# Kernel tuning notes

Hardware: AMD Instinct MI355X
Metric: run time of the kernel (lower is better)

## Reference

```python
import jax, jax.numpy as jnp
import numpy as np

SEQ_LEN = 1024
DIM = 384
QK_DIM = 64
BATCH = 16


def setup_inputs() -> dict:
    key = jax.random.key(0)
    k_x, k_qw, k_qb, k_kw = jax.random.split(key, 4)
    bound = DIM ** (-0.5)
    x = jax.random.normal(k_x, (BATCH, SEQ_LEN, DIM), dtype=jnp.float32)
    # ColumnLinear params: weight [seq_len, out_features, in_features]
    q_weight = jax.random.uniform(k_qw, (SEQ_LEN, QK_DIM, DIM), minval=-bound, maxval=bound, dtype=jnp.float32)
    q_bias = jnp.zeros((SEQ_LEN, QK_DIM), dtype=jnp.float32)  # init zeros; keep as param
    k_weight = jax.random.uniform(k_kw, (SEQ_LEN, QK_DIM, DIM), minval=-bound, maxval=bound, dtype=jnp.float32)
    attn_bias = jnp.zeros((SEQ_LEN, SEQ_LEN), dtype=jnp.float32)
    return {"x": x, "q_weight": q_weight, "q_bias": q_bias, "k_weight": k_weight, "attn_bias": attn_bias}


def reference(x, q_weight, q_bias, k_weight, attn_bias):
    scale = DIM ** (-0.5)  # note: scale uses dim, not qk_dim
    # per-column (untied) linear projections
    q = scale * (jnp.einsum('bnc,ndc->bnd', x, q_weight) + q_bias)  # [B,S,qk]
    k = jnp.einsum('bnc,ndc->bnd', x, k_weight)                     # [B,S,qk]
    attn = jnp.einsum('bnd,bmd->bnm', q, k) + attn_bias             # [B,S,S]
    attn = jax.nn.softmax(attn, axis=-1)
    out = jnp.einsum('bnm,bmc->bnc', attn, x)                       # value = input
    return out, attn
```

## Files before the change

kernel.cpp:

```cpp
#include <hip/hip_runtime.h>

#define B_  16
#define S_  1024
#define D_  384
#define QK_ 64

typedef __attribute__((ext_vector_type(8))) short bf16x8;
typedef __attribute__((ext_vector_type(4))) short bf16x4;
typedef __attribute__((ext_vector_type(4))) float f32x4;

__device__ __forceinline__ short f2bf(float f) {
  union { float f; unsigned u; } v; v.f = f;
  unsigned r = v.u + 0x7FFFu + ((v.u >> 16) & 1u);
  return (short)(r >> 16);
}

__device__ __forceinline__ bf16x4 cvt4(const float4 v) {
  bf16x4 r;
  r[0] = f2bf(v.x); r[1] = f2bf(v.y); r[2] = f2bf(v.z); r[3] = f2bf(v.w);
  return r;
}

__global__ __launch_bounds__(256) void k_proj(
    const float* __restrict__ x, const float* __restrict__ qw,
    const float* __restrict__ qb, const float* __restrict__ kw,
    unsigned short* __restrict__ Qb, unsigned short* __restrict__ Kb) {
  __shared__ __attribute__((aligned(16))) short xs[16 * 392];
  __shared__ __attribute__((aligned(16))) short wsb[128 * 104];

  const int pos  = blockIdx.x;
  const int tid  = threadIdx.x;
  const int lane = tid & 63;
  const int w    = tid >> 6;
  const int col  = lane & 15;
  const int quad = lane >> 4;

#pragma unroll
  for (int r = 0; r < 6; ++r) {
    int li = tid + 256 * r;
    int brow = li / 96, c4 = li % 96;
    float4 v = *(const float4*)&x[(brow * S_ + pos) * D_ + 4 * c4];
    *(bf16x4*)&xs[brow * 392 + 4 * c4] = cvt4(v);
  }

  f32x4 acc0 = {0.f, 0.f, 0.f, 0.f};
  f32x4 acc1 = {0.f, 0.f, 0.f, 0.f};
  const int tt0 = 2 * w, tt1 = 2 * w + 1;

  for (int chunk = 0; chunk < 4; ++chunk) {
    const int c0 = chunk * 96;
    __syncthreads();
#pragma unroll
    for (int r = 0; r < 12; ++r) {
      int li = tid + 256 * r;
      int j = li / 24, c4 = li % 24;
      const float* src = (j < 64)
          ? &qw[(pos * 64 + j) * D_ + c0 + 4 * c4]
          : &kw[(pos * 64 + (j - 64)) * D_ + c0 + 4 * c4];
      *(bf16x4*)&wsb[j * 104 + 4 * c4] = cvt4(*(const float4*)src);
    }
    __syncthreads();
#pragma unroll
    for (int ks = 0; ks < 3; ++ks) {
      bf16x8 aF = *(const bf16x8*)&xs[col * 392 + c0 + ks * 32 + quad * 8];
      bf16x8 b0 = *(const bf16x8*)&wsb[(tt0 * 16 + col) * 104 + ks * 32 + quad * 8];
      bf16x8 b1 = *(const bf16x8*)&wsb[(tt1 * 16 + col) * 104 + ks * 32 + quad * 8];
      acc0 = __builtin_amdgcn_mfma_f32_16x16x32_bf16(aF, b0, acc0, 0, 0, 0);
      acc1 = __builtin_amdgcn_mfma_f32_16x16x32_bf16(aF, b1, acc1, 0, 0, 0);
    }
  }

  const float SCALE = 0.051031036307982884f;
#pragma unroll
  for (int a = 0; a < 2; ++a) {
    const f32x4 acc = a ? acc1 : acc0;
    const int tt = a ? tt1 : tt0;
    const int j = tt * 16 + col;
#pragma unroll
    for (int r = 0; r < 4; ++r) {
      const int brow = quad * 4 + r;
      float v = acc[r];
      if (j < 64) {
        v = SCALE * (v + qb[pos * 64 + j]);
        Qb[(brow * S_ + pos) * QK_ + j] = (unsigned short)f2bf(v);
      } else {
        Kb[(brow * S_ + pos) * QK_ + (j - 64)] = (unsigned short)f2bf(v);
      }
    }
  }
}

__global__ __launch_bounds__(256) void k_logits(
    const unsigned short* __restrict__ Qb, const unsigned short* __restrict__ Kb,
    const float* __restrict__ bias, float* __restrict__ attn) {
  __shared__ __attribute__((aligned(16))) short Qs[64 * 72];
  __shared__ __attribute__((aligned(16))) short Ks[64 * 72];
  const int gid = blockIdx.x;
  const int b = gid >> 8, it = (gid >> 4) & 15, jt = gid & 15;
  const int i0 = it * 64, j0 = jt * 64;
  const int tid = threadIdx.x, lane = tid & 63, w = tid >> 6;
  const int col = lane & 15, quad = lane >> 4;

#pragma unroll
  for (int r = 0; r < 2; ++r) {
    int li = tid + 256 * r;
    int row = li >> 3, q8 = li & 7;
    *(uint4*)&Qs[row * 72 + q8 * 8] =
        *(const uint4*)&Qb[(b * S_ + i0 + row) * QK_ + q8 * 8];
    *(uint4*)&Ks[row * 72 + q8 * 8] =
        *(const uint4*)&Kb[(b * S_ + j0 + row) * QK_ + q8 * 8];
  }
  __syncthreads();

  f32x4 acc[4] = {{0.f,0.f,0.f,0.f},{0.f,0.f,0.f,0.f},
                  {0.f,0.f,0.f,0.f},{0.f,0.f,0.f,0.f}};
#pragma unroll
  for (int ks = 0; ks < 2; ++ks) {
    bf16x8 aF = *(const bf16x8*)&Qs[(w * 16 + col) * 72 + ks * 32 + quad * 8];
#pragma unroll
    for (int s = 0; s < 4; ++s) {
      bf16x8 bF = *(const bf16x8*)&Ks[(s * 16 + col) * 72 + ks * 32 + quad * 8];
      acc[s] = __builtin_amdgcn_mfma_f32_16x16x32_bf16(aF, bF, acc[s], 0, 0, 0);
    }
  }
#pragma unroll
  for (int s = 0; s < 4; ++s) {
    const int j = j0 + s * 16 + col;
#pragma unroll
    for (int r = 0; r < 4; ++r) {
      const int i = i0 + w * 16 + quad * 4 + r;
      attn[(size_t)(b * S_ + i) * S_ + j] = acc[s][r] + bias[i * S_ + j];
    }
  }
}

__global__ __launch_bounds__(256) void k_softmax(float* __restrict__ attn) {
  const int tid = threadIdx.x, lane = tid & 63, w = tid >> 6;
  float* p = attn + (size_t)blockIdx.x * S_;
  float4 v = *(const float4*)&p[tid * 4];
  float m = fmaxf(fmaxf(v.x, v.y), fmaxf(v.z, v.w));
#pragma unroll
  for (int off = 32; off > 0; off >>= 1) m = fmaxf(m, __shfl_xor(m, off));
  __shared__ float redm[4], reds[4];
  if (lane == 0) redm[w] = m;
  __syncthreads();
  m = fmaxf(fmaxf(redm[0], redm[1]), fmaxf(redm[2], redm[3]));
  float4 e;
  e.x = __expf(v.x - m); e.y = __expf(v.y - m);
  e.z = __expf(v.z - m); e.w = __expf(v.w - m);
  float s = e.x + e.y + e.z + e.w;
#pragma unroll
  for (int off = 32; off > 0; off >>= 1) s += __shfl_xor(s, off);
  if (lane == 0) reds[w] = s;
  __syncthreads();
  s = reds[0] + reds[1] + reds[2] + reds[3];
  const float inv = 1.0f / s;
  e.x *= inv; e.y *= inv; e.z *= inv; e.w *= inv;
  *(float4*)&p[tid * 4] = e;
}

__global__ __launch_bounds__(256) void k_out(
    const float* __restrict__ attn, const float* __restrict__ x,
    float* __restrict__ out) {
  __shared__ __attribute__((aligned(16))) short Ps[64 * 40];
  __shared__ __attribute__((aligned(16))) short XsT[128 * 40];
  const int gid = blockIdx.x;
  const int b = gid / 48, r48 = gid % 48;
  const int it = r48 / 3, ct = r48 % 3;
  const int i0 = it * 64, c0 = ct * 128;
  const int tid = threadIdx.x, lane = tid & 63, w = tid >> 6;
  const int col = lane & 15, quad = lane >> 4;

  f32x4 acc[8] = {{0.f,0.f,0.f,0.f},{0.f,0.f,0.f,0.f},{0.f,0.f,0.f,0.f},
                  {0.f,0.f,0.f,0.f},{0.f,0.f,0.f,0.f},{0.f,0.f,0.f,0.f},
                  {0.f,0.f,0.f,0.f},{0.f,0.f,0.f,0.f}};

  for (int j0 = 0; j0 < S_; j0 += 32) {
    __syncthreads();
#pragma unroll
    for (int r = 0; r < 2; ++r) {
      int li = tid + 256 * r;
      int ii = li >> 3, f4 = li & 7;
      float4 v = *(const float4*)&attn[(size_t)(b * S_ + i0 + ii) * S_ + j0 + f4 * 4];
      *(bf16x4*)&Ps[ii * 40 + f4 * 4] = cvt4(v);
    }
#pragma unroll
    for (int r = 0; r < 4; ++r) {
      int li = tid + 256 * r;
      int jj = li >> 5, f4 = li & 31;
      float4 v = *(const float4*)&x[(b * S_ + j0 + jj) * D_ + c0 + f4 * 4];
      XsT[(f4 * 4 + 0) * 40 + jj] = f2bf(v.x);
      XsT[(f4 * 4 + 1) * 40 + jj] = f2bf(v.y);
      XsT[(f4 * 4 + 2) * 40 + jj] = f2bf(v.z);
      XsT[(f4 * 4 + 3) * 40 + jj] = f2bf(v.w);
    }
    __syncthreads();
    bf16x8 aF = *(const bf16x8*)&Ps[(w * 16 + col) * 40 + quad * 8];
#pragma unroll
    for (int s = 0; s < 8; ++s) {
      bf16x8 bF = *(const bf16x8*)&XsT[(s * 16 + col) * 40 + quad * 8];
      acc[s] = __builtin_amdgcn_mfma_f32_16x16x32_bf16(aF, bF, acc[s], 0, 0, 0);
    }
  }
#pragma unroll
  for (int s = 0; s < 8; ++s) {
    const int c = c0 + s * 16 + col;
#pragma unroll
    for (int r = 0; r < 4; ++r) {
      const int i = i0 + w * 16 + quad * 4 + r;
      out[(size_t)(b * S_ + i) * D_ + c] = acc[s][r];
    }
  }
}

extern "C" void kernel_launch(void* const* d_in, const int* in_sizes, int n_in,
                              void* d_out, int out_size, void* d_ws, size_t ws_size,
                              hipStream_t stream) {
  const float* x  = (const float*)d_in[0];
  const float* qw = (const float*)d_in[1];
  const float* qb = (const float*)d_in[2];
  const float* kw = (const float*)d_in[3];
  const float* ab = (const float*)d_in[4];

  float* out  = (float*)d_out;
  float* attn = out + (size_t)B_ * S_ * D_;

  unsigned short* Qb = (unsigned short*)d_ws;
  unsigned short* Kb = Qb + (size_t)B_ * S_ * QK_;

  k_proj   <<<S_,          256, 0, stream>>>(x, qw, qb, kw, Qb, Kb);
  k_logits <<<B_ * 16 * 16, 256, 0, stream>>>(Qb, Kb, ab, attn);
  k_softmax<<<B_ * S_,     256, 0, stream>>>(attn);
  k_out    <<<B_ * 16 * 3, 256, 0, stream>>>(attn, x, out);
}
```

Before: 416.8 us.

## Fuse logits and softmax, pre-transpose x to bf16, feed k_out from bf16 probabilities

The logits and softmax kernels are merged into one kernel that computes a full 16-row slab of scores in registers, applies bias, max, exp and normalization, then writes the fp32 attention plus a bf16 copy. This removes the fp32 attention round trip that the separate softmax pass did. A new prep kernel writes x transposed in bf16, so k_out loads bf16 tiles directly, with no per-iteration conversion or transposing scatter, and uses larger 64x192 tiles. The projection now streams weights straight from global into MFMA operands instead of staging them in LDS. The cost is extra workspace traffic for Xt and Pb and high register pressure in the fused kernel, which holds 16 accumulators.

```diff
diff --git a/kernel.cpp b/kernel.cpp
--- a/kernel.cpp
+++ b/kernel.cpp
@@ -15,10 +15,39 @@
   return (short)(r >> 16);
 }
 
-__device__ __forceinline__ bf16x4 cvt4(const float4 v) {
-  bf16x4 r;
-  r[0] = f2bf(v.x); r[1] = f2bf(v.y); r[2] = f2bf(v.z); r[3] = f2bf(v.w);
+__device__ __forceinline__ bf16x8 cvt8(const float4 a, const float4 b) {
+  bf16x8 r;
+  r[0] = f2bf(a.x); r[1] = f2bf(a.y); r[2] = f2bf(a.z); r[3] = f2bf(a.w);
+  r[4] = f2bf(b.x); r[5] = f2bf(b.y); r[6] = f2bf(b.z); r[7] = f2bf(b.w);
   return r;
+}
+
+__global__ __launch_bounds__(256) void k_prep(
+    const float* __restrict__ x, unsigned short* __restrict__ Xt) {
+  __shared__ __attribute__((aligned(16))) short t[64 * 72];
+  const int gid = blockIdx.x;
+  const int b = gid / 96, r96 = gid % 96;
+  const int jt = r96 / 6, ct = r96 % 6;
+  const int j0 = jt * 64, c0 = ct * 64;
+  const int tid = threadIdx.x;
+#pragma unroll
+  for (int r = 0; r < 4; ++r) {
+    int li = tid + 256 * r;
+    int jj = li >> 4, f4 = li & 15;
+    float4 v = *(const float4*)&x[(size_t)(b * S_ + j0 + jj) * D_ + c0 + f4 * 4];
+    t[(f4 * 4 + 0) * 72 + jj] = f2bf(v.x);
+    t[(f4 * 4 + 1) * 72 + jj] = f2bf(v.y);
+    t[(f4 * 4 + 2) * 72 + jj] = f2bf(v.z);
+    t[(f4 * 4 + 3) * 72 + jj] = f2bf(v.w);
+  }
+  __syncthreads();
+#pragma unroll
+  for (int r = 0; r < 2; ++r) {
+    int li = tid + 256 * r;
+    int cc = li >> 3, q8 = li & 7;
+    *(uint4*)&Xt[(size_t)(b * D_ + c0 + cc) * S_ + j0 + q8 * 8] =
+        *(const uint4*)&t[cc * 72 + q8 * 8];
+  }
 }
 
 __global__ __launch_bounds__(256) void k_proj(
@@ -26,8 +55,6 @@
     const float* __restrict__ qb, const float* __restrict__ kw,
     unsigned short* __restrict__ Qb, unsigned short* __restrict__ Kb) {
   __shared__ __attribute__((aligned(16))) short xs[16 * 392];
-  __shared__ __attribute__((aligned(16))) short wsb[128 * 104];
-
   const int pos  = blockIdx.x;
   const int tid  = threadIdx.x;
   const int lane = tid & 63;
@@ -39,171 +66,192 @@
   for (int r = 0; r < 6; ++r) {
     int li = tid + 256 * r;
     int brow = li / 96, c4 = li % 96;
-    float4 v = *(const float4*)&x[(brow * S_ + pos) * D_ + 4 * c4];
-    *(bf16x4*)&xs[brow * 392 + 4 * c4] = cvt4(v);
-  }
-
-  f32x4 acc0 = {0.f, 0.f, 0.f, 0.f};
-  f32x4 acc1 = {0.f, 0.f, 0.f, 0.f};
-  const int tt0 = 2 * w, tt1 = 2 * w + 1;
-
-  for (int chunk = 0; chunk < 4; ++chunk) {
-    const int c0 = chunk * 96;
-    __syncthreads();
-#pragma unroll
-    for (int r = 0; r < 12; ++r) {
-      int li = tid + 256 * r;
-      int j = li / 24, c4 = li % 24;
-      const float* src = (j < 64)
-          ? &qw[(pos * 64 + j) * D_ + c0 + 4 * c4]
-          : &kw[(pos * 64 + (j - 64)) * D_ + c0 + 4 * c4];
-      *(bf16x4*)&wsb[j * 104 + 4 * c4] = cvt4(*(const float4*)src);
-    }
-    __syncthreads();
-#pragma unroll
-    for (int ks = 0; ks < 3; ++ks) {
-      bf16x8 aF = *(const bf16x8*)&xs[col * 392 + c0 + ks * 32 + quad * 8];
-      bf16x8 b0 = *(const bf16x8*)&wsb[(tt0 * 16 + col) * 104 + ks * 32 + quad * 8];
-      bf16x8 b1 = *(const bf16x8*)&wsb[(tt1 * 16 + col) * 104 + ks * 32 + quad * 8];
-      acc0 = __builtin_amdgcn_mfma_f32_16x16x32_bf16(aF, b0, acc0, 0, 0, 0);
-      acc1 = __builtin_amdgcn_mfma_f32_16x16x32_bf16(aF, b1, acc1, 0, 0, 0);
-    }
+    float4 v = *(const float4*)&x[(size_t)(brow * S_ + pos) * D_ + 4 * c4];
+    bf16x4 c; c[0]=f2bf(v.x); c[1]=f2bf(v.y); c[2]=f2bf(v.z); c[3]=f2bf(v.w);
+    *(bf16x4*)&xs[brow * 392 + 4 * c4] = c;
+  }
+  __syncthreads();
+
+  const bool isQ = (w < 2);
+  const int jt0 = (w & 1) * 2;
+  const float* wp = isQ ? qw : kw;
+  const float* p0 = wp + (size_t)(pos * 64 + jt0 * 16 + col) * D_ + quad * 8;
+  const float* p1 = p0 + 16 * D_;
+
+  f32x4 acc0 = {0.f,0.f,0.f,0.f};
+  f32x4 acc1 = {0.f,0.f,0.f,0.f};
+#pragma unroll 4
+  for (int ks = 0; ks < 12; ++ks) {
+    float4 a0 = *(const float4*)(p0 + ks * 32);
+    float4 a1 = *(const float4*)(p0 + ks * 32 + 4);
+    float4 b0 = *(const float4*)(p1 + ks * 32);
+    float4 b1 = *(const float4*)(p1 + ks * 32 + 4);
+    bf16x8 aF = *(const bf16x8*)&xs[col * 392 + ks * 32 + quad * 8];
+    acc0 = __builtin_amdgcn_mfma_f32_16x16x32_bf16(aF, cvt8(a0, a1), acc0, 0, 0, 0);
+    acc1 = __builtin_amdgcn_mfma_f32_16x16x32_bf16(aF, cvt8(b0, b1), acc1, 0, 0, 0);
   }
 
   const float SCALE = 0.051031036307982884f;
 #pragma unroll
   for (int a = 0; a < 2; ++a) {
     const f32x4 acc = a ? acc1 : acc0;
-    const int tt = a ? tt1 : tt0;
-    const int j = tt * 16 + col;
+    const int j = (jt0 + a) * 16 + col;
 #pragma unroll
     for (int r = 0; r < 4; ++r) {
       const int brow = quad * 4 + r;
       float v = acc[r];
-      if (j < 64) {
+      if (isQ) {
         v = SCALE * (v + qb[pos * 64 + j]);
-        Qb[(brow * S_ + pos) * QK_ + j] = (unsigned short)f2bf(v);
+        Qb[(size_t)(brow * S_ + pos) * QK_ + j] = (unsigned short)f2bf(v);
       } else {
-        Kb[(brow * S_ + pos) * QK_ + (j - 64)] = (unsigned short)f2bf(v);
+        Kb[(size_t)(brow * S_ + pos) * QK_ + j] = (unsigned short)f2bf(v);
       }
     }
   }
 }
 
-__global__ __launch_bounds__(256) void k_logits(
+__global__ __launch_bounds__(256) void k_attn(
     const unsigned short* __restrict__ Qb, const unsigned short* __restrict__ Kb,
-    const float* __restrict__ bias, float* __restrict__ attn) {
-  __shared__ __attribute__((aligned(16))) short Qs[64 * 72];
-  __shared__ __attribute__((aligned(16))) short Ks[64 * 72];
-  const int gid = blockIdx.x;
-  const int b = gid >> 8, it = (gid >> 4) & 15, jt = gid & 15;
-  const int i0 = it * 64, j0 = jt * 64;
+    const float* __restrict__ bias, float* __restrict__ attn,
+    unsigned short* __restrict__ Pb) {
+  __shared__ float rm[4][16];
+  __shared__ float rs[4][16];
+  const int b  = blockIdx.x >> 6;
+  const int i0 = (blockIdx.x & 63) * 16;
   const int tid = threadIdx.x, lane = tid & 63, w = tid >> 6;
   const int col = lane & 15, quad = lane >> 4;
 
-#pragma unroll
-  for (int r = 0; r < 2; ++r) {
-    int li = tid + 256 * r;
-    int row = li >> 3, q8 = li & 7;
-    *(uint4*)&Qs[row * 72 + q8 * 8] =
-        *(const uint4*)&Qb[(b * S_ + i0 + row) * QK_ + q8 * 8];
-    *(uint4*)&Ks[row * 72 + q8 * 8] =
-        *(const uint4*)&Kb[(b * S_ + j0 + row) * QK_ + q8 * 8];
-  }
-  __syncthreads();
-
-  f32x4 acc[4] = {{0.f,0.f,0.f,0.f},{0.f,0.f,0.f,0.f},
-                  {0.f,0.f,0.f,0.f},{0.f,0.f,0.f,0.f}};
-#pragma unroll
-  for (int ks = 0; ks < 2; ++ks) {
-    bf16x8 aF = *(const bf16x8*)&Qs[(w * 16 + col) * 72 + ks * 32 + quad * 8];
-#pragma unroll
-    for (int s = 0; s < 4; ++s) {
-      bf16x8 bF = *(const bf16x8*)&Ks[(s * 16 + col) * 72 + ks * 32 + quad * 8];
-      acc[s] = __builtin_amdgcn_mfma_f32_16x16x32_bf16(aF, bF, acc[s], 0, 0, 0);
-    }
-  }
-#pragma unroll
-  for (int s = 0; s < 4; ++s) {
-    const int j = j0 + s * 16 + col;
-#pragma unroll
-    for (int r = 0; r < 4; ++r) {
-      const int i = i0 + w * 16 + quad * 4 + r;
-      attn[(size_t)(b * S_ + i) * S_ + j] = acc[s][r] + bias[i * S_ + j];
-    }
-  }
-}
-
-__global__ __launch_bounds__(256) void k_softmax(float* __restrict__ attn) {
-  const int tid = threadIdx.x, lane = tid & 63, w = tid >> 6;
-  float* p = attn + (size_t)blockIdx.x * S_;
-  float4 v = *(const float4*)&p[tid * 4];
-  float m = fmaxf(fmaxf(v.x, v.y), fmaxf(v.z, v.w));
-#pragma unroll
-  for (int off = 32; off > 0; off >>= 1) m = fmaxf(m, __shfl_xor(m, off));
-  __shared__ float redm[4], reds[4];
-  if (lane == 0) redm[w] = m;
-  __syncthreads();
-  m = fmaxf(fmaxf(redm[0], redm[1]), fmaxf(redm[2], redm[3]));
-  float4 e;
-  e.x = __expf(v.x - m); e.y = __expf(v.y - m);
-  e.z = __expf(v.z - m); e.w = __expf(v.w - m);
-  float s = e.x + e.y + e.z + e.w;
-#pragma unroll
-  for (int off = 32; off > 0; off >>= 1) s += __shfl_xor(s, off);
-  if (lane == 0) reds[w] = s;
-  __syncthreads();
-  s = reds[0] + reds[1] + reds[2] + reds[3];
-  const float inv = 1.0f / s;
-  e.x *= inv; e.y *= inv; e.z *= inv; e.w *= inv;
-  *(float4*)&p[tid * 4] = e;
+  const unsigned short* qrow = Qb + (size_t)(b * S_ + i0 + col) * QK_;
+  const bf16x8 aF0 = *(const bf16x8*)(qrow);
+  const bf16x8 aF1 = *(const bf16x8*)(qrow + 32);
+  const bf16x8 aQ0 = *(const bf16x8*)(qrow + quad * 8);
+  const bf16x8 aQ1 = *(const bf16x8*)(qrow + 32 + quad * 8);
+  (void)aF0; (void)aF1;
+
+  f32x4 acc[16];
+#pragma unroll
+  for (int s = 0; s < 16; ++s) acc[s] = (f32x4){0.f,0.f,0.f,0.f};
+
+  const unsigned short* kbase = Kb + (size_t)b * S_ * QK_ + (size_t)(w * 256 + col) * QK_;
+#pragma unroll 4
+  for (int s = 0; s < 16; ++s) {
+    const unsigned short* krow = kbase + (size_t)s * 16 * QK_;
+    bf16x8 b0 = *(const bf16x8*)(krow + quad * 8);
+    bf16x8 b1 = *(const bf16x8*)(krow + 32 + quad * 8);
+    acc[s] = __builtin_amdgcn_mfma_f32_16x16x32_bf16(aQ0, b0, acc[s], 0, 0, 0);
+    acc[s] = __builtin_amdgcn_mfma_f32_16x16x32_bf16(aQ1, b1, acc[s], 0, 0, 0);
+  }
+
+  float pm[4] = {-1e30f, -1e30f, -1e30f, -1e30f};
+#pragma unroll 4
+  for (int s = 0; s < 16; ++s) {
+    const int j = w * 256 + s * 16 + col;
+#pragma unroll
+    for (int r = 0; r < 4; ++r) {
+      acc[s][r] += bias[(size_t)(i0 + quad * 4 + r) * S_ + j];
+      pm[r] = fmaxf(pm[r], acc[s][r]);
+    }
+  }
+#pragma unroll
+  for (int m = 1; m < 16; m <<= 1) {
+#pragma unroll
+    for (int r = 0; r < 4; ++r) pm[r] = fmaxf(pm[r], __shfl_xor(pm[r], m));
+  }
+  if (col == 0) {
+#pragma unroll
+    for (int r = 0; r < 4; ++r) rm[w][quad * 4 + r] = pm[r];
+  }
+  __syncthreads();
+#pragma unroll
+  for (int r = 0; r < 4; ++r) {
+    const int i = quad * 4 + r;
+    pm[r] = fmaxf(fmaxf(rm[0][i], rm[1][i]), fmaxf(rm[2][i], rm[3][i]));
+  }
+
+  float ps[4] = {0.f, 0.f, 0.f, 0.f};
+#pragma unroll 4
+  for (int s = 0; s < 16; ++s) {
+#pragma unroll
+    for (int r = 0; r < 4; ++r) {
+      float e = __expf(acc[s][r] - pm[r]);
+      acc[s][r] = e;
+      ps[r] += e;
+    }
+  }
+#pragma unroll
+  for (int m = 1; m < 16; m <<= 1) {
+#pragma unroll
+    for (int r = 0; r < 4; ++r) ps[r] += __shfl_xor(ps[r], m);
+  }
+  if (col == 0) {
+#pragma unroll
+    for (int r = 0; r < 4; ++r) rs[w][quad * 4 + r] = ps[r];
+  }
+  __syncthreads();
+#pragma unroll
+  for (int r = 0; r < 4; ++r) {
+    const int i = quad * 4 + r;
+    ps[r] = 1.0f / (rs[0][i] + rs[1][i] + rs[2][i] + rs[3][i]);
+  }
+
+#pragma unroll 4
+  for (int s = 0; s < 16; ++s) {
+    const int j = w * 256 + s * 16 + col;
+#pragma unroll
+    for (int r = 0; r < 4; ++r) {
+      const size_t row = (size_t)(b * S_ + i0 + quad * 4 + r);
+      float v = acc[s][r] * ps[r];
+      attn[row * S_ + j] = v;
+      Pb[row * S_ + j] = (unsigned short)f2bf(v);
+    }
+  }
 }
 
 __global__ __launch_bounds__(256) void k_out(
-    const float* __restrict__ attn, const float* __restrict__ x,
+    const unsigned short* __restrict__ Pb, const unsigned short* __restrict__ Xt,
     float* __restrict__ out) {
-  __shared__ __attribute__((aligned(16))) short Ps[64 * 40];
-  __shared__ __attribute__((aligned(16))) short XsT[128 * 40];
+  __shared__ __attribute__((aligned(16))) short Ps[64 * 72];
+  __shared__ __attribute__((aligned(16))) short Xs[192 * 72];
   const int gid = blockIdx.x;
-  const int b = gid / 48, r48 = gid % 48;
-  const int it = r48 / 3, ct = r48 % 3;
-  const int i0 = it * 64, c0 = ct * 128;
+  const int b = gid >> 5, r32 = gid & 31;
+  const int it = r32 >> 1, ch = r32 & 1;
+  const int i0 = it * 64, c0 = ch * 192;
   const int tid = threadIdx.x, lane = tid & 63, w = tid >> 6;
   const int col = lane & 15, quad = lane >> 4;
 
-  f32x4 acc[8] = {{0.f,0.f,0.f,0.f},{0.f,0.f,0.f,0.f},{0.f,0.f,0.f,0.f},
-                  {0.f,0.f,0.f,0.f},{0.f,0.f,0.f,0.f},{0.f,0.f,0.f,0.f},
-                  {0.f,0.f,0.f,0.f},{0.f,0.f,0.f,0.f}};
-
-  for (int j0 = 0; j0 < S_; j0 += 32) {
+  f32x4 acc[12];
+#pragma unroll
+  for (int s = 0; s < 12; ++s) acc[s] = (f32x4){0.f,0.f,0.f,0.f};
+
+  for (int j0 = 0; j0 < S_; j0 += 64) {
     __syncthreads();
 #pragma unroll
     for (int r = 0; r < 2; ++r) {
       int li = tid + 256 * r;
-      int ii = li >> 3, f4 = li & 7;
-      float4 v = *(const float4*)&attn[(size_t)(b * S_ + i0 + ii) * S_ + j0 + f4 * 4];
-      *(bf16x4*)&Ps[ii * 40 + f4 * 4] = cvt4(v);
-    }
-#pragma unroll
-    for (int r = 0; r < 4; ++r) {
+      int ii = li >> 3, q8 = li & 7;
+      *(uint4*)&Ps[ii * 72 + q8 * 8] =
+          *(const uint4*)&Pb[(size_t)(b * S_ + i0 + ii) * S_ + j0 + q8 * 8];
+    }
+#pragma unroll
+    for (int r = 0; r < 6; ++r) {
       int li = tid + 256 * r;
-      int jj = li >> 5, f4 = li & 31;
-      float4 v = *(const float4*)&x[(b * S_ + j0 + jj) * D_ + c0 + f4 * 4];
-      XsT[(f4 * 4 + 0) * 40 + jj] = f2bf(v.x);
-      XsT[(f4 * 4 + 1) * 40 + jj] = f2bf(v.y);
-      XsT[(f4 * 4 + 2) * 40 + jj] = f2bf(v.z);
-      XsT[(f4 * 4 + 3) * 40 + jj] = f2bf(v.w);
+      int cc = li >> 3, q8 = li & 7;
+      *(uint4*)&Xs[cc * 72 + q8 * 8] =
+          *(const uint4*)&Xt[(size_t)(b * D_ + c0 + cc) * S_ + j0 + q8 * 8];
     }
     __syncthreads();
-    bf16x8 aF = *(const bf16x8*)&Ps[(w * 16 + col) * 40 + quad * 8];
-#pragma unroll
-    for (int s = 0; s < 8; ++s) {
-      bf16x8 bF = *(const bf16x8*)&XsT[(s * 16 + col) * 40 + quad * 8];
-      acc[s] = __builtin_amdgcn_mfma_f32_16x16x32_bf16(aF, bF, acc[s], 0, 0, 0);
-    }
-  }
-#pragma unroll
-  for (int s = 0; s < 8; ++s) {
+#pragma unroll
+    for (int ks = 0; ks < 2; ++ks) {
+      bf16x8 aF = *(const bf16x8*)&Ps[(w * 16 + col) * 72 + ks * 32 + quad * 8];
+#pragma unroll
+      for (int s = 0; s < 12; ++s) {
+        bf16x8 bF = *(const bf16x8*)&Xs[(s * 16 + col) * 72 + ks * 32 + quad * 8];
+        acc[s] = __builtin_amdgcn_mfma_f32_16x16x32_bf16(aF, bF, acc[s], 0, 0, 0);
+      }
+    }
+  }
+#pragma unroll
+  for (int s = 0; s < 12; ++s) {
     const int c = c0 + s * 16 + col;
 #pragma unroll
     for (int r = 0; r < 4; ++r) {
@@ -227,9 +275,11 @@
 
   unsigned short* Qb = (unsigned short*)d_ws;
   unsigned short* Kb = Qb + (size_t)B_ * S_ * QK_;
-
-  k_proj   <<<S_,          256, 0, stream>>>(x, qw, qb, kw, Qb, Kb);
-  k_logits <<<B_ * 16 * 16, 256, 0, stream>>>(Qb, Kb, ab, attn);
-  k_softmax<<<B_ * S_,     256, 0, stream>>>(attn);
-  k_out    <<<B_ * 16 * 3, 256, 0, stream>>>(attn, x, out);
-}
+  unsigned short* Xt = Kb + (size_t)B_ * S_ * QK_;
+  unsigned short* Pb = Xt + (size_t)B_ * D_ * S_;
+
+  k_prep<<<B_ * 16 * 6, 256, 0, stream>>>(x, Xt);
+  k_proj<<<S_,          256, 0, stream>>>(x, qw, qb, kw, Qb, Kb);
+  k_attn<<<B_ * 64,     256, 0, stream>>>(Qb, Kb, ab, attn, Pb);
+  k_out <<<B_ * 16 * 2, 256, 0, stream>>>(Pb, Xt, out);
+}
```

Measured after the change: 440.5 us. 5.7% more time.
